# Optimization experiments

Hardware: AMD Instinct MI355X
Metric: run time of the kernel (lower is better)

Reference implementation:

```python
import jax, jax.numpy as jnp
import numpy as np

NUM_HEADS = 12   # top-k = num_heads experts selected per token
SWITCHLOSS = 0.1
ZLOSS = 0.001


def setup_inputs() -> dict:
    key = jax.random.key(0)
    ks = jax.random.split(key, 8)
    B, N, C, E, D = 2, 2048, 768, 24, 64
    w = lambda k, shape: (jax.random.normal(k, shape, jnp.float32) * 0.02)
    return {
        "x": jax.random.normal(ks[0], (B, N, C), jnp.float32),
        "w_gate": w(ks[1], (C, E)),
        "W_in": w(ks[2], (E, C, D)),    # per-expert q projection
        "b_in": jnp.zeros((E, D), jnp.float32),
        "W_out": w(ks[3], (E, D, C)),   # per-expert output projection
        "b_out": jnp.zeros((E, C), jnp.float32),
        "W_kv": w(ks[4], (C, 2 * D)),   # shared single-head K/V
        "b_kv": jnp.zeros((2 * D,), jnp.float32),
    }


def reference(x, w_gate, W_in, b_in, W_out, b_out, W_kv, b_kv):
    B, N, C = x.shape
    E, _, D = W_in.shape
    H = NUM_HEADS
    scale = D ** -0.5

    xf = x.reshape(-1, C)                         # [T, C], T = B*N
    # --- top-k gating (k = num_heads) ---
    logits = xf @ w_gate                          # [T, E]
    probs = jax.nn.softmax(logits, axis=-1)
    top_p, idx = jax.lax.top_k(probs, H)          # [T, H]
    gates = top_p / (top_p.sum(-1, keepdims=True) + 1e-6)
    oh = jax.nn.one_hot(idx, E, dtype=x.dtype)    # [T, H, E]
    comb = oh * gates[..., None]                  # gated dispatch/combine weights

    # --- aux losses (switchloss + zloss; cvloss coeff = 0) ---
    dense_gates = comb.sum(1)                     # [T, E]
    freqs = (dense_gates > 0).astype(x.dtype).sum(0)
    p_sum = probs.sum(0)
    switch = E * jnp.sum((p_sum / p_sum.sum()) * (freqs / freqs.sum()))
    z = jnp.mean(jax.nn.logsumexp(logits, axis=1) ** 2)
    aux_loss = SWITCHLOSS * switch + ZLOSS * z

    # --- MoE map: per-token q via selected experts (no gate multiply) ---
    q_all = jnp.einsum('tc,ecd->ted', xf, W_in) + b_in     # [T, E, D]
    q = jnp.take_along_axis(q_all, idx[..., None], axis=1)  # [T, H, D]
    q = q.reshape(B, N, H, D)

    # --- shared-KV attention (multi-query style) ---
    kv = x @ W_kv + b_kv
    k, v = jnp.split(kv, 2, axis=-1)              # [B, N, D] each
    attn = jnp.einsum('bihd,bjd->bhij', q, k) * scale
    attn = jax.nn.softmax(attn, axis=-1)
    o = jnp.einsum('bhij,bjd->bihd', attn, v).reshape(-1, H, D)  # [T, H, D]

    # --- MoE reduce: gated combine through per-expert output projections ---
    xe = jnp.einsum('the,thd->ted', comb, o)      # [T, E, D] gated dispatch
    out = jnp.einsum('ted,edc->tc', xe, W_out) + jnp.einsum('the,ec->tc', comb, b_out)
    return out.reshape(B, N, C), aux_loss
```

## Files before the change

kernel.cpp:

```cpp
#include <hip/hip_runtime.h>
#include <hip/hip_bf16.h>

#define T_  4096
#define Bb  2
#define Nn  2048
#define Cc  768
#define Ee  24
#define Dd  64
#define Hh  12
#define KR  1600
#define KS  16
#define KC  48
#define NB2 1024
#define SCL 0.18033688f

typedef __attribute__((ext_vector_type(8))) short bf16x8;
typedef __attribute__((ext_vector_type(4))) short bf16x4;
typedef __attribute__((ext_vector_type(4))) float f32x4;

__device__ __forceinline__ unsigned short f2bf(float f) {
  union { float f; unsigned int i; } u; u.f = f;
  unsigned int r = u.i + 0x7FFFu + ((u.i >> 16) & 1u);
  return (unsigned short)(r >> 16);
}

__device__ __forceinline__ void gload16(const void* g, void* l) {
  __builtin_amdgcn_global_load_lds(
      (const __attribute__((address_space(1))) void*)g,
      (__attribute__((address_space(3))) void*)l, 16, 0, 0);
}

__global__ __launch_bounds__(256) void convert_all_kernel(
    const float* __restrict__ W_in, const float* __restrict__ W_out,
    const float* __restrict__ b_out, const float* __restrict__ W_kv,
    unsigned short* __restrict__ BqT, unsigned short* __restrict__ BrT,
    unsigned short* __restrict__ BkvT)
{
  __shared__ float ls[64 * 129];
  const int bid = blockIdx.x, tid = threadIdx.x;
  if (bid < 288) {
    const int e = bid / 12, c0 = (bid % 12) * 64;
    #pragma unroll
    for (int i = 0; i < 16; ++i) {
      int L = tid + i * 256, c = L >> 6, d = L & 63;
      ls[c * 65 + d] = W_in[(size_t)e * Cc * Dd + (size_t)(c0 + c) * Dd + d];
    }
    __syncthreads();
    #pragma unroll
    for (int i = 0; i < 16; ++i) {
      int L = tid + i * 256, d = L >> 6, c = L & 63;
      BqT[(size_t)(e * Dd + d) * Cc + c0 + c] = f2bf(ls[c * 65 + d]);
    }
  } else if (bid < 888) {
    const int i2 = bid - 288;
    const int k0 = (i2 / 12) * 32, n0 = (i2 % 12) * 64;
    #pragma unroll
    for (int i = 0; i < 8; ++i) {
      int L = tid + i * 256, k = L >> 6, n = L & 63;
      int kk = k0 + k;
      float v = (kk < 1536) ? W_out[(size_t)kk * Cc + n0 + n]
              : (kk < 1560) ? b_out[(size_t)(kk - 1536) * Cc + n0 + n] : 0.f;
      ls[k * 65 + n] = v;
    }
    __syncthreads();
    #pragma unroll
    for (int i = 0; i < 8; ++i) {
      int L = tid + i * 256, n = L >> 5, k = L & 31;
      BrT[(size_t)(n0 + n) * KR + k0 + k] = f2bf(ls[k * 65 + n]);
    }
  } else {
    const int c0 = (bid - 888) * 64;
    #pragma unroll
    for (int i = 0; i < 32; ++i) {
      int L = tid + i * 256, c = L >> 7, j = L & 127;
      ls[c * 129 + j] = W_kv[(size_t)(c0 + c) * 128 + j];
    }
    __syncthreads();
    #pragma unroll
    for (int i = 0; i < 32; ++i) {
      int L = tid + i * 256, j = L >> 6, c = L & 63;
      BkvT[(size_t)j * Cc + c0 + c] = f2bf(ls[c * 129 + j]);
    }
  }
}

template<int MODE>
__global__ __launch_bounds__(256) void gemm_bt_kernel(
    const unsigned short* __restrict__ A, const unsigned short* __restrict__ BT,
    const float* __restrict__ bias, const float* __restrict__ bias2,
    void* __restrict__ Cout, void* __restrict__ Cout2, void* __restrict__ Cout3,
    int K, int ldc)
{
  constexpr int BM = 64, BN = 64, MI = 2, NI = 2;
  __shared__ __align__(16) unsigned short As[2][BM * 64];
  __shared__ __align__(16) unsigned short Bs[2][BN * 64];
  const int tid = threadIdx.x, w = tid >> 6, lane = tid & 63;
  const int quad = lane >> 4, nl = lane & 15;
  const int m0 = blockIdx.x * BM, n0 = blockIdx.y * BN;
  const int mw = (w & 1) * 32, nw = (w >> 1) * 32;

  f32x4 acc[MI][NI];
  #pragma unroll
  for (int i = 0; i < MI; ++i)
    #pragma unroll
    for (int j = 0; j < NI; ++j) acc[i][j] = (f32x4){0.f, 0.f, 0.f, 0.f};

  const int sr  = lane >> 3;
  const int cbd = (lane & 7) ^ sr;
  const int xl  = nl & 15 & 7;
  const int ca0 = (quad ^ xl) * 8;
  const int ca1 = ((quad + 4) ^ xl) * 8;

  const unsigned short* abase = A + (size_t)(m0 + w * 16 + sr) * K + cbd * 8;
  const unsigned short* bbase = BT + (size_t)(n0 + w * 16 + sr) * K + cbd * 8;

  auto STAGE = [&](int bi, int k0) {
    #pragma unroll
    for (int i = 0; i < 2; ++i) {
      gload16(abase + (size_t)(i * 8) * K + k0, &As[bi][(w * 16 + i * 8) * 64]);
      gload16(bbase + (size_t)(i * 8) * K + k0, &Bs[bi][(w * 16 + i * 8) * 64]);
    }
  };

  const int nt = K / 64;
  STAGE(0, 0);
  __syncthreads();
  for (int t = 0; t < nt; ++t) {
    const int cur = t & 1;
    if (t + 1 < nt) STAGE(cur ^ 1, (t + 1) * 64);

    bf16x8 af0[MI], af1[MI], bf0[NI], bf1[NI];
    #pragma unroll
    for (int mi = 0; mi < MI; ++mi) {
      const unsigned short* ar = &As[cur][(mw + mi * 16 + nl) * 64];
      af0[mi] = *(const bf16x8*)(ar + ca0);
      af1[mi] = *(const bf16x8*)(ar + ca1);
    }
    #pragma unroll
    for (int ni = 0; ni < NI; ++ni) {
      const unsigned short* br = &Bs[cur][(nw + ni * 16 + nl) * 64];
      bf0[ni] = *(const bf16x8*)(br + ca0);
      bf1[ni] = *(const bf16x8*)(br + ca1);
    }
    #pragma unroll
    for (int mi = 0; mi < MI; ++mi)
      #pragma unroll
      for (int ni = 0; ni < NI; ++ni) {
        acc[mi][ni] = __builtin_amdgcn_mfma_f32_16x16x32_bf16(
            af0[mi], bf0[ni], acc[mi][ni], 0, 0, 0);
        acc[mi][ni] = __builtin_amdgcn_mfma_f32_16x16x32_bf16(
            af1[mi], bf1[ni], acc[mi][ni], 0, 0, 0);
      }

    __syncthreads();
  }

  #pragma unroll
  for (int mi = 0; mi < MI; ++mi) {
    int rowb = m0 + mw + mi * 16 + quad * 4;
    int bb = rowb >> 11, nn = rowb & (Nn - 1);
    #pragma unroll
    for (int ni = 0; ni < NI; ++ni) {
      int col = n0 + nw + ni * 16 + nl;
      if (MODE == 0) {
        #pragma unroll
        for (int reg = 0; reg < 4; ++reg)
          ((float*)Cout)[(size_t)(rowb + reg) * ldc + col] = acc[mi][ni][reg];
      } else {
        if (col < 1536) {
          float bv = bias[col];
          #pragma unroll
          for (int reg = 0; reg < 4; ++reg)
            ((unsigned short*)Cout)[(size_t)(rowb + reg) * 1536 + col] =
                f2bf((acc[mi][ni][reg] + bv) * SCL);
        } else {
          int c2 = col - 1536;
          float bv = bias2[c2];
          if (c2 < Dd) {
            #pragma unroll
            for (int reg = 0; reg < 4; ++reg)
              ((unsigned short*)Cout2)[((size_t)bb * Nn + nn + reg) * Dd + c2] =
                  f2bf(acc[mi][ni][reg] + bv);
          } else {
            int p6 = nn & 63;
            int np = (nn & ~63) | (p6 & 0x23)
                   | (((p6 >> 4) & 1) << 2) | (((p6 >> 2) & 3) << 3);
            ushort4 v;
            v.x = f2bf(acc[mi][ni][0] + bv);
            v.y = f2bf(acc[mi][ni][1] + bv);
            v.z = f2bf(acc[mi][ni][2] + bv);
            v.w = f2bf(acc[mi][ni][3] + bv);
            *(ushort4*)((unsigned short*)Cout3 +
                        ((size_t)bb * Dd + (c2 - Dd)) * Nn + np) = v;
          }
        }
      }
    }
  }
}

#define XPAD 52
__global__ __launch_bounds__(256) void gate1_kernel(
    const float* __restrict__ x, const float* __restrict__ wg,
    float* __restrict__ partial, unsigned short* __restrict__ xb)
{
  __shared__ __align__(16) float xs[256 * XPAD];
  __shared__ __align__(16) float wsT[Ee * KC];
  const int tid = threadIdx.x;
  const int t0 = blockIdx.x * 256;
  const int s = blockIdx.y, k0 = s * KC;

  #pragma unroll
  for (int i = 0; i < 12; ++i) {
    int f = tid + i * 256;
    int token = f / 12, j = f % 12;
    size_t gofs = (size_t)(t0 + token) * Cc + k0 + j * 4;
    float4 v = *(const float4*)&x[gofs];
    *(float4*)&xs[token * XPAD + j * 4] = v;
    ushort4 o;
    o.x = f2bf(v.x); o.y = f2bf(v.y); o.z = f2bf(v.z); o.w = f2bf(v.w);
    *(ushort4*)&xb[gofs] = o;
  }
  for (int i = tid; i < Ee * KC; i += 256)
    wsT[(i % Ee) * KC + i / Ee] = wg[k0 * Ee + i];
  __syncthreads();

  float xr[KC];
  #pragma unroll
  for (int kg = 0; kg < KC / 4; ++kg)
    *(float4*)&xr[kg * 4] = *(const float4*)&xs[tid * XPAD + kg * 4];

  float acc[Ee];
  #pragma unroll
  for (int e = 0; e < Ee; ++e) acc[e] = 0.f;
  #pragma unroll
  for (int e = 0; e < Ee; ++e) {
    #pragma unroll
    for (int kg = 0; kg < KC / 4; ++kg) {
      float4 wv = *(const float4*)&wsT[e * KC + kg * 4];
      acc[e] += xr[kg * 4 + 0] * wv.x + xr[kg * 4 + 1] * wv.y
              + xr[kg * 4 + 2] * wv.z + xr[kg * 4 + 3] * wv.w;
    }
  }

  float* dst = partial + ((size_t)(t0 + tid) * KS + s) * Ee;
  #pragma unroll
  for (int eg = 0; eg < Ee / 4; ++eg)
    *(float4*)&dst[eg * 4] = *(float4*)&acc[eg * 4];
}

__global__ __launch_bounds__(256) void gate2_kernel(
    const float* __restrict__ partial,
    int* __restrict__ idx, float* __restrict__ gate, float* __restrict__ bstats)
{
  __shared__ float xls[4][KS * Ee];
  __shared__ float sacc[49];
  const int tid = threadIdx.x;
  const int w = tid >> 6, lane = tid & 63;
  const int t = blockIdx.x * 4 + w;

  if (tid < 49) sacc[tid] = 0.f;

  const float* p = partial + (size_t)t * (KS * Ee);
  #pragma unroll
  for (int i = 0; i < 6; ++i) xls[w][lane + i * 64] = p[lane + i * 64];

  float logit = -1e30f;
  if (lane < Ee) {
    float acc = 0.f;
    #pragma unroll
    for (int s = 0; s < KS; ++s) acc += xls[w][s * Ee + lane];
    logit = acc;
  }
  float m = logit;
  for (int o = 32; o; o >>= 1) m = fmaxf(m, __shfl_xor(m, o));
  float pr = (lane < Ee) ? expf(logit - m) : 0.f;
  float s = pr;
  for (int o = 32; o; o >>= 1) s += __shfl_xor(s, o);
  float prob = pr / s;
  float lse = m + logf(s);

  bool sel = false;
  float my_p = 0.f; int my_e = -1;
  for (int h = 0; h < Hh; ++h) {
    float v = (lane < Ee && !sel) ? prob : -1.f;
    int ix = lane;
    for (int o = 32; o; o >>= 1) {
      float ov = __shfl_xor(v, o); int oi = __shfl_xor(ix, o);
      if (ov > v || (ov == v && oi < ix)) { v = ov; ix = oi; }
    }
    if (lane == ix) sel = true;
    if (lane == h) { my_p = v; my_e = ix; }
  }
  float gsum = (lane < Hh) ? my_p : 0.f;
  for (int o = 32; o; o >>= 1) gsum += __shfl_xor(gsum, o);
  if (lane < Hh) {
    idx[t * Hh + lane] = my_e;
    gate[t * Hh + lane] = my_p / (gsum + 1e-6f);
  }

  __syncthreads();
  if (lane < Ee) atomicAdd(&sacc[lane], prob);
  if (lane < Hh) atomicAdd(&sacc[24 + my_e], 1.0f);
  if (lane == 0) atomicAdd(&sacc[48], lse * lse);
  __syncthreads();
  if (tid < 49) bstats[(size_t)tid * NB2 + blockIdx.x] = sacc[tid];
}

__global__ __launch_bounds__(256, 3) void attn_kernel(
    const unsigned short* __restrict__ qallb, const int* __restrict__ idx,
    const unsigned short* __restrict__ kbuf, const unsigned short* __restrict__ vtbuf,
    float* __restrict__ opart, float* __restrict__ lpart)
{
  __shared__ __align__(16) unsigned short ksl[3][64 * 64];
  __shared__ __align__(16) unsigned short vtl[3][64 * 64];

  const int tid = threadIdx.x;
  const int w = tid >> 6, lane = tid & 63;
  const int quad = lane >> 4, nl = lane & 15;
  const int bh = blockIdx.y;
  const int b = bh / Hh, h = bh - b * Hh;
  const int qw = blockIdx.x * 64 + w * 16;

  const int tq = b * Nn + qw + nl;
  const int eq = idx[tq * Hh + h];
  const unsigned short* qrow = qallb + (size_t)tq * (Ee * Dd) + eq * Dd + quad * 8;
  const bf16x8 qB0 = *(const bf16x8*)(qrow);
  const bf16x8 qB1 = *(const bf16x8*)(qrow + 32);

  f32x4 acc[4];
  #pragma unroll
  for (int dg = 0; dg < 4; ++dg) acc[dg] = (f32x4){0.f, 0.f, 0.f, 0.f};
  float l = 0.f;

  const int sr  = lane >> 3;
  const int cbd = (lane & 7) ^ sr;
  const int xl  = nl & 7;
  const int ca0 = (quad ^ xl) * 8;
  const int ca1 = ((quad + 4) ^ xl) * 8;

  const unsigned short* kgbase =
      kbuf + ((size_t)b * Nn + w * 16 + sr) * Dd + cbd * 8;
  const unsigned short* vgbase =
      vtbuf + ((size_t)b * Dd + w * 16 + sr) * Nn + cbd * 8;

  auto STAGE = [&](int bi, int t) {
    const int j0 = t * 64;
    #pragma unroll
    for (int i = 0; i < 2; ++i) {
      gload16(kgbase + (size_t)(j0 + i * 8) * Dd, &ksl[bi][(w * 16 + i * 8) * 64]);
      gload16(vgbase + (size_t)(i * 8) * Nn + j0, &vtl[bi][(w * 16 + i * 8) * 64]);
    }
  };

  auto COMPUTE = [&](const unsigned short* ks_, const unsigned short* vt_) {
    __builtin_amdgcn_s_setprio(1);
    bf16x4 pf[4];
    #pragma unroll
    for (int kg = 0; kg < 4; ++kg) {
      const unsigned short* kr = ks_ + (kg * 16 + nl) * 64;
      bf16x8 a0 = *(const bf16x8*)(kr + ca0);
      bf16x8 a1 = *(const bf16x8*)(kr + ca1);
      f32x4 c = {0.f, 0.f, 0.f, 0.f};
      c = __builtin_amdgcn_mfma_f32_16x16x32_bf16(a0, qB0, c, 0, 0, 0);
      c = __builtin_amdgcn_mfma_f32_16x16x32_bf16(a1, qB1, c, 0, 0, 0);
      float p0 = __builtin_amdgcn_exp2f(c[0]);
      float p1 = __builtin_amdgcn_exp2f(c[1]);
      float p2 = __builtin_amdgcn_exp2f(c[2]);
      float p3 = __builtin_amdgcn_exp2f(c[3]);
      l += (p0 + p1) + (p2 + p3);
      union { __hip_bfloat162 h2[2]; bf16x4 v; } pk;
      pk.h2[0] = __float22bfloat162_rn(float2{p0, p1});
      pk.h2[1] = __float22bfloat162_rn(float2{p2, p3});
      pf[kg] = pk.v;
    }
    bf16x8 pb0 = __builtin_shufflevector(pf[0], pf[1], 0, 1, 2, 3, 4, 5, 6, 7);
    bf16x8 pb1 = __builtin_shufflevector(pf[2], pf[3], 0, 1, 2, 3, 4, 5, 6, 7);
    #pragma unroll
    for (int dg = 0; dg < 4; ++dg) {
      const unsigned short* vrow = vt_ + (dg * 16 + nl) * 64;
      bf16x8 v0 = *(const bf16x8*)(vrow + ca0);
      bf16x8 v1 = *(const bf16x8*)(vrow + ca1);
      acc[dg] = __builtin_amdgcn_mfma_f32_16x16x32_bf16(v0, pb0, acc[dg], 0, 0, 0);
      acc[dg] = __builtin_amdgcn_mfma_f32_16x16x32_bf16(v1, pb1, acc[dg], 0, 0, 0);
    }
    __builtin_amdgcn_s_setprio(0);
  };

  STAGE(0, 0);
  STAGE(1, 1);
  #pragma unroll 1
  for (int t = 0; t < 30; t += 3) {
    STAGE(2, t + 2);
    asm volatile("s_waitcnt vmcnt(8)" ::: "memory");
    __builtin_amdgcn_s_barrier();
    __builtin_amdgcn_sched_barrier(0);
    COMPUTE(ksl[0], vtl[0]);
    __builtin_amdgcn_sched_barrier(0);
    asm volatile("" ::: "memory");
    __builtin_amdgcn_s_barrier();

    STAGE(0, t + 3);
    asm volatile("s_waitcnt vmcnt(8)" ::: "memory");
    __builtin_amdgcn_s_barrier();
    __builtin_amdgcn_sched_barrier(0);
    COMPUTE(ksl[1], vtl[1]);
    __builtin_amdgcn_sched_barrier(0);
    asm volatile("" ::: "memory");
    __builtin_amdgcn_s_barrier();

    STAGE(1, t + 4);
    asm volatile("s_waitcnt vmcnt(8)" ::: "memory");
    __builtin_amdgcn_s_barrier();
    __builtin_amdgcn_sched_barrier(0);
    COMPUTE(ksl[2], vtl[2]);
    __builtin_amdgcn_sched_barrier(0);
    asm volatile("" ::: "memory");
    __builtin_amdgcn_s_barrier();
  }
  asm volatile("s_waitcnt vmcnt(4)" ::: "memory");
  __builtin_amdgcn_s_barrier();
  __builtin_amdgcn_sched_barrier(0);
  COMPUTE(ksl[0], vtl[0]);
  __builtin_amdgcn_sched_barrier(0);
  asm volatile("s_waitcnt vmcnt(0)" ::: "memory");
  __builtin_amdgcn_s_barrier();
  __builtin_amdgcn_sched_barrier(0);
  COMPUTE(ksl[1], vtl[1]);

  float lg = l;
  lg += __shfl_xor(lg, 16);
  lg += __shfl_xor(lg, 32);
  if (lane < 16)
    lpart[(size_t)bh * Nn + qw + nl] = lg;
  float* orow = opart + ((size_t)bh * Nn + qw + nl) * Dd + quad * 4;
  #pragma unroll
  for (int dg = 0; dg < 4; ++dg) {
    float4 o;
    o.x = acc[dg][0]; o.y = acc[dg][1];
    o.z = acc[dg][2]; o.w = acc[dg][3];
    *(float4*)(orow + dg * 16) = o;
  }
}

__global__ __launch_bounds__(256) void scatter_kernel(
    const float* __restrict__ opart, const float* __restrict__ lpart,
    const int* __restrict__ idx, const float* __restrict__ gate,
    unsigned short* __restrict__ xeg)
{
  __shared__ int   sel[Ee];
  __shared__ float glh[Hh];
  __shared__ float gg[Hh];
  const int t = blockIdx.x, b = t >> 11, nn = t & (Nn - 1);
  const int tid = threadIdx.x;
  if (tid < Ee) sel[tid] = -1;
  __syncthreads();
  if (tid < Hh) {
    int e = idx[t * Hh + tid];
    sel[e] = tid;
    float g = gate[t * Hh + tid];
    gg[tid] = g;
    size_t row = (size_t)(b * Hh + tid) * Nn + nn;
    glh[tid] = g / lpart[row];
  }
  __syncthreads();
  for (int c = tid; c < KR; c += 256) {
    float v = 0.f;
    if (c < 1536) {
      int e = c >> 6, h = sel[e];
      if (h >= 0) {
        size_t oofs = ((size_t)(b * Hh + h) * Nn + nn) * Dd + (c & 63);
        v = glh[h] * opart[oofs];
      }
    } else if (c < 1560) {
      int h = sel[c - 1536];
      if (h >= 0) v = gg[h];
    }
    xeg[(size_t)t * KR + c] = f2bf(v);
  }
}

__global__ __launch_bounds__(256) void aux1_kernel(
    const float* __restrict__ bstats, float* __restrict__ stats2)
{
  __shared__ float r[4];
  const int j = blockIdx.x, tid = threadIdx.x;
  float4 v = *(const float4*)&bstats[(size_t)j * NB2 + tid * 4];
  float s = (v.x + v.y) + (v.z + v.w);
  for (int o = 32; o; o >>= 1) s += __shfl_xor(s, o);
  if ((tid & 63) == 0) r[tid >> 6] = s;
  __syncthreads();
  if (tid == 0) stats2[j] = (r[0] + r[1]) + (r[2] + r[3]);
}

__global__ void aux2_kernel(const float* __restrict__ stats2,
                            float* __restrict__ out, int out_size)
{
  const int lane = threadIdx.x;
  float a = (lane < Ee) ? stats2[lane] : 0.f;
  float b = (lane < Ee) ? stats2[24 + lane] : 0.f;
  float pt = a, ft = b, sw = a * b;
  for (int o = 32; o; o >>= 1) {
    pt += __shfl_xor(pt, o); ft += __shfl_xor(ft, o); sw += __shfl_xor(sw, o);
  }
  if (lane == 0) {
    float sswitch = (float)Ee * sw / (pt * ft);
    float z = stats2[48] * (1.0f / (float)T_);
    out[out_size - 1] = 0.1f * sswitch + 0.001f * z;
  }
}

extern "C" void kernel_launch(void* const* d_in, const int* in_sizes, int n_in,
                              void* d_out, int out_size, void* d_ws, size_t ws_size,
                              hipStream_t stream)
{
  const float* x     = (const float*)d_in[0];
  const float* wg    = (const float*)d_in[1];
  const float* W_in  = (const float*)d_in[2];
  const float* b_in  = (const float*)d_in[3];
  const float* W_out = (const float*)d_in[4];
  const float* b_out = (const float*)d_in[5];
  const float* W_kv  = (const float*)d_in[6];
  const float* b_kv  = (const float*)d_in[7];
  float* out = (float*)d_out;

  char* ws = (char*)d_ws;
  size_t off = 0;
  auto carve = [&](size_t bytes) -> void* {
    void* p = ws + off;
    off = (off + bytes + 255) & ~(size_t)255;
    return p;
  };
  int*            idx    = (int*)           carve((size_t)T_ * Hh * 4);
  float*          gate   = (float*)         carve((size_t)T_ * Hh * 4);
  float*          bstats = (float*)         carve((size_t)49 * NB2 * 4);
  float*          stats2 = (float*)         carve(256);
  float*          lpart  = (float*)         carve((size_t)Bb * Hh * Nn * 4);
  float*          lgate  = (float*)         carve((size_t)T_ * KS * Ee * 4);
  unsigned short* xb     = (unsigned short*)carve((size_t)T_ * Cc * 2);
  unsigned short* BqkvT  = (unsigned short*)carve((size_t)(Ee * Dd + 128) * Cc * 2);
  unsigned short* BkvT   = BqkvT + (size_t)Ee * Dd * Cc;
  unsigned short* BrT    = (unsigned short*)carve((size_t)Cc * KR * 2);
  unsigned short* kbuf   = (unsigned short*)carve((size_t)T_ * Dd * 2);
  unsigned short* vtbuf  = (unsigned short*)carve((size_t)T_ * Dd * 2);
  unsigned short* qallb  = (unsigned short*)carve((size_t)T_ * Ee * Dd * 2);
  float*          opart  = (float*)         carve((size_t)Bb * Hh * Nn * Dd * 4);
  unsigned short* xeg    = (unsigned short*)carve((size_t)T_ * KR * 2);

  convert_all_kernel<<<900, 256, 0, stream>>>(
      W_in, W_out, b_out, W_kv, BqkvT, BrT, BkvT);

  gate1_kernel<<<dim3(T_ / 256, KS), 256, 0, stream>>>(x, wg, lgate, xb);
  gate2_kernel<<<NB2, 256, 0, stream>>>(lgate, idx, gate, bstats);

  gemm_bt_kernel<1><<<dim3(T_ / 64, 26), 256, 0, stream>>>(
      xb, BqkvT, b_in, b_kv, qallb, kbuf, vtbuf, Cc, 1536);

  attn_kernel<<<dim3(Nn / 64, Bb * Hh), 256, 0, stream>>>(
      qallb, idx, kbuf, vtbuf, opart, lpart);

  scatter_kernel<<<T_, 256, 0, stream>>>(opart, lpart, idx, gate, xeg);

  gemm_bt_kernel<0><<<dim3(T_ / 64, Cc / 64), 256, 0, stream>>>(
      xeg, BrT, nullptr, nullptr, out, nullptr, nullptr, KR, Cc);

  aux1_kernel<<<49, 256, 0, stream>>>(bstats, stats2);
  aux2_kernel<<<1, 64, 0, stream>>>(stats2, out, out_size);
}
```

Before: 191.1 us.

## Fuse gated scatter into attention epilogue and zero xeg in gate kernel

Removes the separate scatter kernel and the fp32 opart/lpart intermediates. The attention epilogue now normalizes by the softmax denominator, multiplies by the gate, converts to bf16 and writes directly into the expert-dispatched xeg row. The gate kernel pre-zeroes each xeg row and writes the dense gate columns used for the bias term. This saves a kernel launch and a full fp32 round trip through global memory. In exchange it relies on ordering between the zeroing pass in gate2 and the attention writes, and on each token's 12 selected experts covering disjoint slots.

```diff
diff --git a/kernel.cpp b/kernel.cpp
--- a/kernel.cpp
+++ b/kernel.cpp
@@ -17,6 +17,7 @@
 typedef __attribute__((ext_vector_type(8))) short bf16x8;
 typedef __attribute__((ext_vector_type(4))) short bf16x4;
 typedef __attribute__((ext_vector_type(4))) float f32x4;
+typedef __attribute__((ext_vector_type(8))) unsigned short u16x8;
 
 __device__ __forceinline__ unsigned short f2bf(float f) {
   union { float f; unsigned int i; } u; u.f = f;
@@ -107,7 +108,7 @@
 
   const int sr  = lane >> 3;
   const int cbd = (lane & 7) ^ sr;
-  const int xl  = nl & 15 & 7;
+  const int xl  = nl & 7;
   const int ca0 = (quad ^ xl) * 8;
   const int ca1 = ((quad + 4) ^ xl) * 8;
 
@@ -251,19 +252,30 @@
 
 __global__ __launch_bounds__(256) void gate2_kernel(
     const float* __restrict__ partial,
-    int* __restrict__ idx, float* __restrict__ gate, float* __restrict__ bstats)
+    int* __restrict__ idx, float* __restrict__ gate, float* __restrict__ bstats,
+    unsigned short* __restrict__ xeg)
 {
   __shared__ float xls[4][KS * Ee];
   __shared__ float sacc[49];
+  __shared__ unsigned short dens[4][64];
   const int tid = threadIdx.x;
   const int w = tid >> 6, lane = tid & 63;
   const int t = blockIdx.x * 4 + w;
 
   if (tid < 49) sacc[tid] = 0.f;
+  dens[w][lane] = 0;
 
   const float* p = partial + (size_t)t * (KS * Ee);
   #pragma unroll
   for (int i = 0; i < 6; ++i) xls[w][lane + i * 64] = p[lane + i * 64];
+
+  {
+    u16x8 z = (u16x8){0, 0, 0, 0, 0, 0, 0, 0};
+    unsigned short* xrow = xeg + (size_t)t * KR;
+    #pragma unroll
+    for (int i = 0; i < 3; ++i)
+      *(u16x8*)&xrow[(lane + i * 64) * 8] = z;
+  }
 
   float logit = -1e30f;
   if (lane < Ee) {
@@ -294,23 +306,30 @@
   }
   float gsum = (lane < Hh) ? my_p : 0.f;
   for (int o = 32; o; o >>= 1) gsum += __shfl_xor(gsum, o);
+  float gval = my_p / (gsum + 1e-6f);
   if (lane < Hh) {
     idx[t * Hh + lane] = my_e;
-    gate[t * Hh + lane] = my_p / (gsum + 1e-6f);
+    gate[t * Hh + lane] = gval;
   }
 
   __syncthreads();
   if (lane < Ee) atomicAdd(&sacc[lane], prob);
-  if (lane < Hh) atomicAdd(&sacc[24 + my_e], 1.0f);
+  if (lane < Hh) {
+    atomicAdd(&sacc[24 + my_e], 1.0f);
+    dens[w][my_e] = f2bf(gval);
+  }
   if (lane == 0) atomicAdd(&sacc[48], lse * lse);
   __syncthreads();
   if (tid < 49) bstats[(size_t)tid * NB2 + blockIdx.x] = sacc[tid];
+
+  xeg[(size_t)t * KR + 1536 + lane] = dens[w][lane];
 }
 
 __global__ __launch_bounds__(256, 3) void attn_kernel(
     const unsigned short* __restrict__ qallb, const int* __restrict__ idx,
+    const float* __restrict__ gate,
     const unsigned short* __restrict__ kbuf, const unsigned short* __restrict__ vtbuf,
-    float* __restrict__ opart, float* __restrict__ lpart)
+    unsigned short* __restrict__ xeg)
 {
   __shared__ __align__(16) unsigned short ksl[3][64 * 64];
   __shared__ __align__(16) unsigned short vtl[3][64 * 64];
@@ -431,52 +450,16 @@
   float lg = l;
   lg += __shfl_xor(lg, 16);
   lg += __shfl_xor(lg, 32);
-  if (lane < 16)
-    lpart[(size_t)bh * Nn + qw + nl] = lg;
-  float* orow = opart + ((size_t)bh * Nn + qw + nl) * Dd + quad * 4;
+  const float scale = gate[tq * Hh + h] / lg;
+  unsigned short* xrow = xeg + (size_t)tq * KR + eq * Dd + quad * 4;
   #pragma unroll
   for (int dg = 0; dg < 4; ++dg) {
-    float4 o;
-    o.x = acc[dg][0]; o.y = acc[dg][1];
-    o.z = acc[dg][2]; o.w = acc[dg][3];
-    *(float4*)(orow + dg * 16) = o;
-  }
-}
-
-__global__ __launch_bounds__(256) void scatter_kernel(
-    const float* __restrict__ opart, const float* __restrict__ lpart,
-    const int* __restrict__ idx, const float* __restrict__ gate,
-    unsigned short* __restrict__ xeg)
-{
-  __shared__ int   sel[Ee];
-  __shared__ float glh[Hh];
-  __shared__ float gg[Hh];
-  const int t = blockIdx.x, b = t >> 11, nn = t & (Nn - 1);
-  const int tid = threadIdx.x;
-  if (tid < Ee) sel[tid] = -1;
-  __syncthreads();
-  if (tid < Hh) {
-    int e = idx[t * Hh + tid];
-    sel[e] = tid;
-    float g = gate[t * Hh + tid];
-    gg[tid] = g;
-    size_t row = (size_t)(b * Hh + tid) * Nn + nn;
-    glh[tid] = g / lpart[row];
-  }
-  __syncthreads();
-  for (int c = tid; c < KR; c += 256) {
-    float v = 0.f;
-    if (c < 1536) {
-      int e = c >> 6, h = sel[e];
-      if (h >= 0) {
-        size_t oofs = ((size_t)(b * Hh + h) * Nn + nn) * Dd + (c & 63);
-        v = glh[h] * opart[oofs];
-      }
-    } else if (c < 1560) {
-      int h = sel[c - 1536];
-      if (h >= 0) v = gg[h];
-    }
-    xeg[(size_t)t * KR + c] = f2bf(v);
+    ushort4 v;
+    v.x = f2bf(acc[dg][0] * scale);
+    v.y = f2bf(acc[dg][1] * scale);
+    v.z = f2bf(acc[dg][2] * scale);
+    v.w = f2bf(acc[dg][3] * scale);
+    *(ushort4*)(xrow + dg * 16) = v;
   }
 }
 
@@ -535,7 +518,6 @@
   float*          gate   = (float*)         carve((size_t)T_ * Hh * 4);
   float*          bstats = (float*)         carve((size_t)49 * NB2 * 4);
   float*          stats2 = (float*)         carve(256);
-  float*          lpart  = (float*)         carve((size_t)Bb * Hh * Nn * 4);
   float*          lgate  = (float*)         carve((size_t)T_ * KS * Ee * 4);
   unsigned short* xb     = (unsigned short*)carve((size_t)T_ * Cc * 2);
   unsigned short* BqkvT  = (unsigned short*)carve((size_t)(Ee * Dd + 128) * Cc * 2);
@@ -544,22 +526,19 @@
   unsigned short* kbuf   = (unsigned short*)carve((size_t)T_ * Dd * 2);
   unsigned short* vtbuf  = (unsigned short*)carve((size_t)T_ * Dd * 2);
   unsigned short* qallb  = (unsigned short*)carve((size_t)T_ * Ee * Dd * 2);
-  float*          opart  = (float*)         carve((size_t)Bb * Hh * Nn * Dd * 4);
   unsigned short* xeg    = (unsigned short*)carve((size_t)T_ * KR * 2);
 
   convert_all_kernel<<<900, 256, 0, stream>>>(
       W_in, W_out, b_out, W_kv, BqkvT, BrT, BkvT);
 
   gate1_kernel<<<dim3(T_ / 256, KS), 256, 0, stream>>>(x, wg, lgate, xb);
-  gate2_kernel<<<NB2, 256, 0, stream>>>(lgate, idx, gate, bstats);
+  gate2_kernel<<<NB2, 256, 0, stream>>>(lgate, idx, gate, bstats, xeg);
 
   gemm_bt_kernel<1><<<dim3(T_ / 64, 26), 256, 0, stream>>>(
       xb, BqkvT, b_in, b_kv, qallb, kbuf, vtbuf, Cc, 1536);
 
   attn_kernel<<<dim3(Nn / 64, Bb * Hh), 256, 0, stream>>>(
-      qallb, idx, kbuf, vtbuf, opart, lpart);
-
-  scatter_kernel<<<T_, 256, 0, stream>>>(opart, lpart, idx, gate, xeg);
+      qallb, idx, gate, kbuf, vtbuf, xeg);
 
   gemm_bt_kernel<0><<<dim3(T_ / 64, Cc / 64), 256, 0, stream>>>(
       xeg, BrT, nullptr, nullptr, out, nullptr, nullptr, KR, Cc);
```

After: 183.8 us. 1.04x faster.
